# Kernel tuning notes

Hardware: AMD Instinct MI355X
Metric: run time of the kernel (lower is better)

Reference implementation:

```python
import jax, jax.numpy as jnp
import numpy as np

BN_EPS = 1e-3  # Keras BatchNormalization default epsilon


def _conv_block(x, k):
    """Per-task conv (stride 2, pad 1) -> ReLU -> BatchNorm (center/scale=False, training).

    x: [B, E, H, W, Cin]  (B tasks, E examples per task)
    k: [B, kh, kw, Cin, Cout]  per-task kernel
    """
    def conv_one(xe, kt):  # xe: [E,H,W,Cin], kt: [kh,kw,Cin,Cout]
        return jax.lax.conv_general_dilated(
            xe, kt, window_strides=(2, 2), padding=[(1, 1), (1, 1)],
            dimension_numbers=('NHWC', 'HWIO', 'NHWC'))
    y = jax.nn.relu(jax.vmap(conv_one)(x, k))  # [B,E,H',W',Cout]
    # BatchNorm in training mode: moments over all axes except channels
    m = jnp.mean(y, axis=(0, 1, 2, 3))
    v = jnp.var(y, axis=(0, 1, 2, 3))
    return (y - m) * jax.lax.rsqrt(v + BN_EPS)


def setup_inputs() -> dict:
    key = jax.random.key(0)
    ks = jax.random.split(key, 6)
    B, E, H, C, O = 64, 64, 28, 64, 20
    return {
        'x': jax.random.normal(ks[0], (B, E, H, H, 1), dtype=jnp.float32),
        'k1': jax.random.normal(ks[1], (B, 3, 3, 1, C), dtype=jnp.float32) * 0.1,
        'k2': jax.random.normal(ks[2], (B, 3, 3, C, C), dtype=jnp.float32) * 0.05,
        'k3': jax.random.normal(ks[3], (B, 3, 3, C, C), dtype=jnp.float32) * 0.05,
        'k4': jax.random.normal(ks[4], (B, 3, 3, C, C), dtype=jnp.float32) * 0.05,
        'w_ro': jax.random.normal(ks[5], (B, C, O), dtype=jnp.float32) * 0.1,
    }


def reference(x, k1, k2, k3, k4, w_ro):
    h = _conv_block(x, k1)   # [B,E,14,14,C]
    h = _conv_block(h, k2)   # [B,E,7,7,C]
    h = _conv_block(h, k3)   # [B,E,4,4,C]
    h = _conv_block(h, k4)   # [B,E,2,2,C]
    # MaxPooling2D with pool size == full spatial extent -> global spatial max
    feat = jnp.max(h, axis=(2, 3))  # [B,E,C]
    # per-task readout matmul: [B,E,H] x [B,H,O] -> [B,E,O]
    return jnp.einsum('beh,bho->beo', feat, w_ro)
```

## Files before the change

kernel.cpp:

```cpp
#include <hip/hip_runtime.h>

#define BN_EPS 1e-3f

typedef __attribute__((ext_vector_type(8))) short bf16x8;
typedef __attribute__((ext_vector_type(16))) float floatx16;
typedef unsigned short u16;

__device__ __forceinline__ u16 f2bf(float f) {
  unsigned u = __float_as_uint(f);
  u += 0x7fffu + ((u >> 16) & 1u);
  return (u16)(u >> 16);
}
__device__ __forceinline__ float bf2f(u16 h) {
  return __uint_as_float(((unsigned)h) << 16);
}

static constexpr int NSHARD = 64;

__global__ __launch_bounds__(256) void conv1_kernel(
    const float* __restrict__ x, const float* __restrict__ k1,
    u16* __restrict__ y1, float* __restrict__ statsSh)
{
  __shared__ float xp[900];
  __shared__ float w1[576];
  __shared__ float red[256];

  const int be = blockIdx.x, b = be >> 6, tid = threadIdx.x;

  for (int i = tid; i < 900; i += 256) xp[i] = 0.f;
  for (int i = tid; i < 576; i += 256) w1[i] = k1[(size_t)b * 576 + i];
  __syncthreads();
  for (int i = tid; i < 784; i += 256) {
    const int r = i / 28, cc = i - 28 * r;
    xp[(r + 1) * 30 + (cc + 1)] = x[(size_t)be * 784 + i];
  }
  __syncthreads();

  const int c = tid & 63;
  float wr[9];
#pragma unroll
  for (int t = 0; t < 9; ++t) wr[t] = w1[t * 64 + c];

  float sum = 0.f, ss = 0.f;
  for (int pix = tid >> 6; pix < 196; pix += 4) {
    const int oy = pix / 14, ox = pix - 14 * oy;
    const float* xb = &xp[(2 * oy) * 30 + 2 * ox];
    float acc = 0.f;
#pragma unroll
    for (int ky = 0; ky < 3; ++ky)
#pragma unroll
      for (int kx = 0; kx < 3; ++kx)
        acc = fmaf(xb[ky * 30 + kx], wr[ky * 3 + kx], acc);
    const float v = fmaxf(acc, 0.f);
    y1[((size_t)be * 196 + pix) * 64 + c] = f2bf(v);
    sum += v;
    ss = fmaf(v, v, ss);
  }

  red[tid] = sum;
  __syncthreads();
  if (tid < 64)
    atomicAdd(&statsSh[(blockIdx.x & (NSHARD - 1)) * 128 + tid],
              red[tid] + red[tid + 64] + red[tid + 128] + red[tid + 192]);
  __syncthreads();
  red[tid] = ss;
  __syncthreads();
  if (tid < 64)
    atomicAdd(&statsSh[(blockIdx.x & (NSHARD - 1)) * 128 + 64 + tid],
              red[tid] + red[tid + 64] + red[tid + 128] + red[tid + 192]);
}

__global__ __launch_bounds__(256) void fold_kernel(
    const float* __restrict__ W, const float* __restrict__ statsSh, float invN,
    u16* __restrict__ Wf, float* __restrict__ biasCls)
{
  __shared__ float T[64 * 68];
  __shared__ float P[256];
  __shared__ float s1[64], t1[64];
  __shared__ float tbS[64];

  const int b = blockIdx.x / 3, sg = blockIdx.x % 3;
  const int tid = threadIdx.x;

  {
    const int g = tid >> 7, cidx = tid & 127;
    float acc = 0.f;
    for (int k = 0; k < NSHARD / 2; ++k)
      acc += statsSh[(g * (NSHARD / 2) + k) * 128 + cidx];
    P[tid] = acc;
  }
  __syncthreads();
  if (tid < 64) {
    const float m = (P[tid] + P[tid + 128]) * invN;
    const float var = fmaf(-m, m, (P[64 + tid] + P[192 + tid]) * invN);
    const float s = rsqrtf(var + BN_EPS);
    s1[tid] = s;
    t1[tid] = -m * s;
  }
  __syncthreads();

  const int cin = tid >> 2, q0 = (tid & 3) * 16;
  const int cout = tid >> 2, ci0 = (tid & 3) * 16;
  for (int s = sg * 3; s < sg * 3 + 3; ++s) {
    if (tid < 64) tbS[tid] = 0.f;
    const float* ss = W + ((size_t)b * 9 + s) * 4096;
#pragma unroll
    for (int q = 0; q < 16; q += 4) {
      const float4 v = *(const float4*)(ss + cin * 64 + q0 + q);
      T[(q0 + q + 0) * 68 + cin] = v.x;
      T[(q0 + q + 1) * 68 + cin] = v.y;
      T[(q0 + q + 2) * 68 + cin] = v.z;
      T[(q0 + q + 3) * 68 + cin] = v.w;
    }
    __syncthreads();
    alignas(16) u16 tmp[16];
    float tb = 0.f;
#pragma unroll
    for (int j = 0; j < 16; ++j) {
      const float wv = T[cout * 68 + ci0 + j];
      tmp[j] = f2bf(wv * s1[ci0 + j]);
      tb = fmaf(t1[ci0 + j], wv, tb);
    }
    u16* dst = Wf + ((size_t)b * 9 + s) * 4096 + cout * 64 + ci0;
    *(uint4*)dst       = *(uint4*)&tmp[0];
    *(uint4*)(dst + 8) = *(uint4*)&tmp[8];
    atomicAdd(&tbS[cout], tb);
    __syncthreads();
    if (tid < 64) {
      const int ky = s / 3, kx = s % 3;
      const float tv = tbS[tid];
#pragma unroll
      for (int cls = 0; cls < 9; ++cls) {
        const int ry = cls / 3, rx = cls % 3;
        const bool valid = !((ry == 1 && ky == 0) || (ry == 2 && ky == 2) ||
                             (rx == 1 && kx == 0) || (rx == 2 && kx == 2));
        if (valid) atomicAdd(&biasCls[(size_t)b * 576 + cls * 64 + tid], tv);
      }
    }
    __syncthreads();
  }
}

template <int Hin, int Hout, int G>
__global__ __launch_bounds__(256) void conv_gemm_kernel(
    const u16* __restrict__ yin, const u16* __restrict__ Wf,
    const float* __restrict__ biasCls, u16* __restrict__ yout,
    float* __restrict__ statsSh)
{
  constexpr int PPI  = Hout * Hout;
  constexpr int ROWS = G * PPI;
  constexpr int BPT  = 64 / G;
  constexpr int LDA  = 68;

  __shared__ __align__(16) u16 AS[128 * LDA];
  __shared__ __align__(16) u16 BtS[64 * LDA];
  __shared__ float biasS[576];
  __shared__ float redsum[64], redss[64];

  const int b = blockIdx.x / BPT;
  const int e0 = (blockIdx.x % BPT) * G;
  const int tid = threadIdx.x, lane = tid & 63, wave = tid >> 6;

  for (int i = tid; i < 576; i += 256) biasS[i] = biasCls[(size_t)b * 576 + i];
  if (tid < 64) { redsum[tid] = 0.f; redss[tid] = 0.f; }

  const int arow = tid >> 1, ci0 = (tid & 1) * 32;
  const bool rowOk = arow < ROWS;
  const int g = rowOk ? arow / PPI : 0;
  const int pp = rowOk ? arow % PPI : 0;
  const int oy = pp / Hout, ox = pp % Hout;
  const size_t inBase = ((size_t)(b * 64 + e0 + g)) * (Hin * Hin) * 64;

  const int bco = tid >> 2, bci = (tid & 3) * 16;
  const u16* wbase = Wf + (size_t)b * 9 * 4096 + bco * 64 + bci;

  uint4 pa0, pa1, pa2, pa3, pb0, pb1;
  auto loadSlice = [&](int s) {
    const int ky = s / 3, kx = s % 3;
    const int iy = 2 * oy - 1 + ky, ix = 2 * ox - 1 + kx;
    if (rowOk && (unsigned)iy < (unsigned)Hin && (unsigned)ix < (unsigned)Hin) {
      const u16* src = yin + inBase + (size_t)(iy * Hin + ix) * 64 + ci0;
      pa0 = *(const uint4*)(src);
      pa1 = *(const uint4*)(src + 8);
      pa2 = *(const uint4*)(src + 16);
      pa3 = *(const uint4*)(src + 24);
    } else {
      pa0 = pa1 = pa2 = pa3 = uint4{0, 0, 0, 0};
    }
    const u16* wsl = wbase + s * 4096;
    pb0 = *(const uint4*)wsl;
    pb1 = *(const uint4*)(wsl + 8);
  };

  const int m0 = wave * 32;
  const int l31 = lane & 31;
  const int kq = (lane >> 5) * 8;

  floatx16 acc0, acc1;
#pragma unroll
  for (int r = 0; r < 16; ++r) { acc0[r] = 0.f; acc1[r] = 0.f; }

  loadSlice(0);
#pragma unroll
  for (int s = 0; s < 9; ++s) {
    *(uint4*)&AS[arow * LDA + ci0]      = pa0;
    *(uint4*)&AS[arow * LDA + ci0 + 8]  = pa1;
    *(uint4*)&AS[arow * LDA + ci0 + 16] = pa2;
    *(uint4*)&AS[arow * LDA + ci0 + 24] = pa3;
    *(uint4*)&BtS[bco * LDA + bci]     = pb0;
    *(uint4*)&BtS[bco * LDA + bci + 8] = pb1;
    __syncthreads();
    if (s < 8) loadSlice(s + 1);
#pragma unroll
    for (int kk = 0; kk < 4; ++kk) {
      const int ko = kk * 16 + kq;
      bf16x8 a  = *(const bf16x8*)&AS[(m0 + l31) * LDA + ko];
      bf16x8 b0 = *(const bf16x8*)&BtS[l31 * LDA + ko];
      bf16x8 b1 = *(const bf16x8*)&BtS[(32 + l31) * LDA + ko];
      acc0 = __builtin_amdgcn_mfma_f32_32x32x16_bf16(a, b0, acc0, 0, 0, 0);
      acc1 = __builtin_amdgcn_mfma_f32_32x32x16_bf16(a, b1, acc1, 0, 0, 0);
    }
    __syncthreads();
  }

  float ls0 = 0.f, lss0 = 0.f, ls1 = 0.f, lss1 = 0.f;
  const int col0 = l31, col1 = 32 + l31;
  const int rb = m0 + 4 * (lane >> 5);
#pragma unroll
  for (int r = 0; r < 16; ++r) {
    const int rw = rb + (r & 3) + 8 * (r >> 2);
    if (rw < ROWS) {
      const int re = rw / PPI, pr = rw % PPI;
      const int ooy = pr / Hout, oox = pr % Hout;
      const int ry = (ooy == 0) ? 1 : ((2 * ooy + 1 >= Hin) ? 2 : 0);
      const int rx = (oox == 0) ? 1 : ((2 * oox + 1 >= Hin) ? 2 : 0);
      const int cls = ry * 3 + rx;
      const size_t ob = ((size_t)(b * 64 + e0 + re) * PPI + pr) * 64;
      const float v0 = fmaxf(acc0[r] + biasS[cls * 64 + col0], 0.f);
      const float v1 = fmaxf(acc1[r] + biasS[cls * 64 + col1], 0.f);
      yout[ob + col0] = f2bf(v0);
      yout[ob + col1] = f2bf(v1);
      ls0 += v0; lss0 = fmaf(v0, v0, lss0);
      ls1 += v1; lss1 = fmaf(v1, v1, lss1);
    }
  }
  atomicAdd(&redsum[col0], ls0);
  atomicAdd(&redss[col0], lss0);
  atomicAdd(&redsum[col1], ls1);
  atomicAdd(&redss[col1], lss1);
  __syncthreads();
  if (tid < 64) {
    const int sh = blockIdx.x & (NSHARD - 1);
    atomicAdd(&statsSh[sh * 128 + tid], redsum[tid]);
    atomicAdd(&statsSh[sh * 128 + 64 + tid], redss[tid]);
  }
}

__global__ __launch_bounds__(256) void readout_kernel(
    const u16* __restrict__ y4, const float* __restrict__ w_ro,
    const float* __restrict__ statsSh, float invN, float* __restrict__ outp)
{
  __shared__ float wl[64 * 20];
  __shared__ float feat[64 * 64];
  __shared__ float P[256];
  __shared__ float sArr[64], tArr[64];

  const int b = blockIdx.x, tid = threadIdx.x;

  {
    const int g = tid >> 7, cidx = tid & 127;
    float acc = 0.f;
    for (int k = 0; k < NSHARD / 2; ++k)
      acc += statsSh[(g * (NSHARD / 2) + k) * 128 + cidx];
    P[tid] = acc;
  }
  for (int i = tid; i < 1280; i += 256) wl[i] = w_ro[(size_t)b * 1280 + i];
  __syncthreads();
  if (tid < 64) {
    const float m = (P[tid] + P[tid + 128]) * invN;
    const float var = fmaf(-m, m, (P[64 + tid] + P[192 + tid]) * invN);
    const float s = rsqrtf(var + BN_EPS);
    sArr[tid] = s;
    tArr[tid] = -m * s;
  }
  __syncthreads();

  {
    const int e = tid & 63;
    for (int c = tid >> 6; c < 64; c += 4) {
      const u16* p4 = y4 + ((size_t)(b * 64 + e) * 4) * 64 + c;
      const float v = fmaxf(fmaxf(bf2f(p4[0]), bf2f(p4[64])),
                            fmaxf(bf2f(p4[128]), bf2f(p4[192])));
      feat[c * 64 + e] = fmaf(v, sArr[c], tArr[c]);
    }
  }
  __syncthreads();

  const int e = tid >> 2, og = (tid & 3) * 5;
  float acc[5] = {0.f, 0.f, 0.f, 0.f, 0.f};
  for (int c = 0; c < 64; ++c) {
    const float f = feat[c * 64 + e];
#pragma unroll
    for (int j = 0; j < 5; ++j) acc[j] = fmaf(f, wl[c * 20 + og + j], acc[j]);
  }
#pragma unroll
  for (int j = 0; j < 5; ++j)
    outp[((size_t)b * 64 + e) * 20 + og + j] = acc[j];
}

extern "C" void kernel_launch(void* const* d_in, const int* in_sizes, int n_in,
                              void* d_out, int out_size, void* d_ws, size_t ws_size,
                              hipStream_t stream) {
  (void)in_sizes; (void)n_in; (void)out_size; (void)ws_size;
  const float* x   = (const float*)d_in[0];
  const float* k1  = (const float*)d_in[1];
  const float* k2  = (const float*)d_in[2];
  const float* k3  = (const float*)d_in[3];
  const float* k4  = (const float*)d_in[4];
  const float* wro = (const float*)d_in[5];
  float* out = (float*)d_out;
  char* ws = (char*)d_ws;

  float* stats = (float*)ws;
  float* bias2 = (float*)(ws + 131072);
  float* bias3 = bias2 + 36864;
  float* bias4 = bias3 + 36864;
  u16* k2f = (u16*)(ws + 131072 + 442368);
  u16* k3f = k2f + (size_t)2359296;
  u16* k4f = k3f + (size_t)2359296;
  u16* y2 = k4f + (size_t)2359296;
  u16* y1 = y2 + (size_t)12845056;
  u16* y3 = y1;
  u16* y4 = y3 + (size_t)4194304;

  float* st1 = stats;
  float* st2 = stats + 8192;
  float* st3 = stats + 16384;
  float* st4 = stats + 24576;

  hipMemsetAsync(stats, 0, 131072 + 442368, stream);

  conv1_kernel<<<4096, 256, 0, stream>>>(x, k1, y1, st1);
  fold_kernel<<<192, 256, 0, stream>>>(k2, st1, 1.f / 802816.f, k2f, bias2);
  conv_gemm_kernel<14, 7, 2><<<2048, 256, 0, stream>>>(y1, k2f, bias2, y2, st2);
  fold_kernel<<<192, 256, 0, stream>>>(k3, st2, 1.f / 200704.f, k3f, bias3);
  conv_gemm_kernel<7, 4, 8><<<512, 256, 0, stream>>>(y2, k3f, bias3, y3, st3);
  fold_kernel<<<192, 256, 0, stream>>>(k4, st3, 1.f / 65536.f, k4f, bias4);
  conv_gemm_kernel<4, 2, 32><<<128, 256, 0, stream>>>(y3, k4f, bias4, y4, st4);
  readout_kernel<<<64, 256, 0, stream>>>(y4, wro, st4, 1.f / 16384.f, out);
}
```

Before: 309.9 us.

## Stage whole input images in LDS for conv GEMMs and register-tile conv1

```diff
diff --git a/kernel.cpp b/kernel.cpp
--- a/kernel.cpp
+++ b/kernel.cpp
@@ -17,60 +17,74 @@
 
 static constexpr int NSHARD = 64;
 
-__global__ __launch_bounds__(256) void conv1_kernel(
+__global__ __launch_bounds__(256) void conv1_k(
     const float* __restrict__ x, const float* __restrict__ k1,
     u16* __restrict__ y1, float* __restrict__ statsSh)
 {
-  __shared__ float xp[900];
-  __shared__ float w1[576];
-  __shared__ float red[256];
+  __shared__ float xp[30 * 32];
+  __shared__ float w1s[576];
+  __shared__ float redsum[64], redss[64];
 
   const int be = blockIdx.x, b = be >> 6, tid = threadIdx.x;
 
-  for (int i = tid; i < 900; i += 256) xp[i] = 0.f;
-  for (int i = tid; i < 576; i += 256) w1[i] = k1[(size_t)b * 576 + i];
+  for (int i = tid; i < 960; i += 256) xp[i] = 0.f;
+  for (int i = tid; i < 576; i += 256) w1s[i] = k1[(size_t)b * 576 + i];
+  if (tid < 64) { redsum[tid] = 0.f; redss[tid] = 0.f; }
   __syncthreads();
   for (int i = tid; i < 784; i += 256) {
-    const int r = i / 28, cc = i - 28 * r;
-    xp[(r + 1) * 30 + (cc + 1)] = x[(size_t)be * 784 + i];
-  }
-  __syncthreads();
-
-  const int c = tid & 63;
-  float wr[9];
-#pragma unroll
-  for (int t = 0; t < 9; ++t) wr[t] = w1[t * 64 + c];
-
-  float sum = 0.f, ss = 0.f;
-  for (int pix = tid >> 6; pix < 196; pix += 4) {
-    const int oy = pix / 14, ox = pix - 14 * oy;
-    const float* xb = &xp[(2 * oy) * 30 + 2 * ox];
-    float acc = 0.f;
+    const int r = i / 28, c = i - 28 * r;
+    xp[(r + 1) * 32 + (c + 1)] = x[(size_t)be * 784 + i];
+  }
+  __syncthreads();
+
+  if (tid < 224) {
+    const int oy = tid >> 4, cg = (tid & 15) * 4;
+    float w[4][9];
+#pragma unroll
+    for (int cc = 0; cc < 4; ++cc)
+#pragma unroll
+      for (int t = 0; t < 9; ++t) w[cc][t] = w1s[t * 64 + cg + cc];
+
+    float xr[3][29];
 #pragma unroll
     for (int ky = 0; ky < 3; ++ky)
 #pragma unroll
-      for (int kx = 0; kx < 3; ++kx)
-        acc = fmaf(xb[ky * 30 + kx], wr[ky * 3 + kx], acc);
-    const float v = fmaxf(acc, 0.f);
-    y1[((size_t)be * 196 + pix) * 64 + c] = f2bf(v);
-    sum += v;
-    ss = fmaf(v, v, ss);
-  }
-
-  red[tid] = sum;
-  __syncthreads();
-  if (tid < 64)
-    atomicAdd(&statsSh[(blockIdx.x & (NSHARD - 1)) * 128 + tid],
-              red[tid] + red[tid + 64] + red[tid + 128] + red[tid + 192]);
-  __syncthreads();
-  red[tid] = ss;
-  __syncthreads();
-  if (tid < 64)
-    atomicAdd(&statsSh[(blockIdx.x & (NSHARD - 1)) * 128 + 64 + tid],
-              red[tid] + red[tid + 64] + red[tid + 128] + red[tid + 192]);
-}
-
-__global__ __launch_bounds__(256) void fold_kernel(
+      for (int j = 0; j < 29; ++j) xr[ky][j] = xp[(2 * oy + ky) * 32 + j];
+
+    float sum[4] = {0.f, 0.f, 0.f, 0.f}, ss[4] = {0.f, 0.f, 0.f, 0.f};
+#pragma unroll
+    for (int ox = 0; ox < 14; ++ox) {
+      alignas(8) u16 o[4];
+#pragma unroll
+      for (int cc = 0; cc < 4; ++cc) {
+        float a = 0.f;
+#pragma unroll
+        for (int ky = 0; ky < 3; ++ky)
+#pragma unroll
+          for (int kx = 0; kx < 3; ++kx)
+            a = fmaf(xr[ky][2 * ox + kx], w[cc][ky * 3 + kx], a);
+        const float v = fmaxf(a, 0.f);
+        o[cc] = f2bf(v);
+        sum[cc] += v;
+        ss[cc] = fmaf(v, v, ss[cc]);
+      }
+      *(uint2*)&y1[((size_t)be * 196 + oy * 14 + ox) * 64 + cg] = *(uint2*)o;
+    }
+#pragma unroll
+    for (int cc = 0; cc < 4; ++cc) {
+      atomicAdd(&redsum[cg + cc], sum[cc]);
+      atomicAdd(&redss[cg + cc], ss[cc]);
+    }
+  }
+  __syncthreads();
+  if (tid < 64) {
+    const int sh = be & (NSHARD - 1);
+    atomicAdd(&statsSh[sh * 128 + tid], redsum[tid]);
+    atomicAdd(&statsSh[sh * 128 + 64 + tid], redss[tid]);
+  }
+}
+
+__global__ __launch_bounds__(256) void foldw_k(
     const float* __restrict__ W, const float* __restrict__ statsSh, float invN,
     u16* __restrict__ Wf, float* __restrict__ biasCls)
 {
@@ -142,90 +156,94 @@
 }
 
 template <int Hin, int Hout, int G>
-__global__ __launch_bounds__(256) void conv_gemm_kernel(
+__device__ __forceinline__ void conv_core(
     const u16* __restrict__ yin, const u16* __restrict__ Wf,
     const float* __restrict__ biasCls, u16* __restrict__ yout,
-    float* __restrict__ statsSh)
+    float* __restrict__ statsSh, int blk)
 {
   constexpr int PPI  = Hout * Hout;
   constexpr int ROWS = G * PPI;
   constexpr int BPT  = 64 / G;
-  constexpr int LDA  = 68;
-
-  __shared__ __align__(16) u16 AS[128 * LDA];
-  __shared__ __align__(16) u16 BtS[64 * LDA];
+  constexpr int MR   = G * Hin * Hin;
+  constexpr int ZR   = MR;
+
+  __shared__ __align__(16) u16 mapS[(MR + 1) * 72];
+  __shared__ __align__(16) u16 Bb[2][64 * 72];
   __shared__ float biasS[576];
   __shared__ float redsum[64], redss[64];
 
-  const int b = blockIdx.x / BPT;
-  const int e0 = (blockIdx.x % BPT) * G;
+  const int b = blk / BPT, e0 = (blk % BPT) * G;
   const int tid = threadIdx.x, lane = tid & 63, wave = tid >> 6;
 
   for (int i = tid; i < 576; i += 256) biasS[i] = biasCls[(size_t)b * 576 + i];
   if (tid < 64) { redsum[tid] = 0.f; redss[tid] = 0.f; }
-
-  const int arow = tid >> 1, ci0 = (tid & 1) * 32;
-  const bool rowOk = arow < ROWS;
-  const int g = rowOk ? arow / PPI : 0;
-  const int pp = rowOk ? arow % PPI : 0;
+  if (tid < 8) *(uint4*)&mapS[ZR * 72 + tid * 8] = uint4{0, 0, 0, 0};
+
+  {
+    const u16* src = yin + (size_t)(b * 64 + e0) * (Hin * Hin) * 64;
+    for (int ch = tid; ch < MR * 8; ch += 256) {
+      const int r = ch >> 3, c8 = ch & 7;
+      *(uint4*)&mapS[r * 72 + c8 * 8] = *(const uint4*)(src + ch * 8);
+    }
+  }
+
+  const int bco = tid >> 2, bci = (tid & 3) * 16;
+  const u16* wb = Wf + (size_t)b * 9 * 4096 + bco * 64 + bci;
+  {
+    uint4 b0 = *(const uint4*)wb;
+    uint4 b1 = *(const uint4*)(wb + 8);
+    *(uint4*)&Bb[0][bco * 72 + bci]     = b0;
+    *(uint4*)&Bb[0][bco * 72 + bci + 8] = b1;
+  }
+
+  const int m0 = (wave & 1) * 32, n0 = (wave >> 1) * 32;
+  const int l31 = lane & 31, kq = (lane >> 5) * 8;
+  const int lrow = m0 + l31;
+  const bool rv = lrow < ROWS;
+  const int img = rv ? lrow / PPI : 0;
+  const int pp  = rv ? lrow % PPI : 0;
   const int oy = pp / Hout, ox = pp % Hout;
-  const size_t inBase = ((size_t)(b * 64 + e0 + g)) * (Hin * Hin) * 64;
-
-  const int bco = tid >> 2, bci = (tid & 3) * 16;
-  const u16* wbase = Wf + (size_t)b * 9 * 4096 + bco * 64 + bci;
-
-  uint4 pa0, pa1, pa2, pa3, pb0, pb1;
-  auto loadSlice = [&](int s) {
+
+  floatx16 acc;
+#pragma unroll
+  for (int r = 0; r < 16; ++r) acc[r] = 0.f;
+
+  __syncthreads();
+
+#pragma unroll
+  for (int s = 0; s < 9; ++s) {
+    uint4 nb0, nb1;
+    if (s < 8) {
+      const u16* wsl = wb + (s + 1) * 4096;
+      nb0 = *(const uint4*)wsl;
+      nb1 = *(const uint4*)(wsl + 8);
+    }
     const int ky = s / 3, kx = s % 3;
-    const int iy = 2 * oy - 1 + ky, ix = 2 * ox - 1 + kx;
-    if (rowOk && (unsigned)iy < (unsigned)Hin && (unsigned)ix < (unsigned)Hin) {
-      const u16* src = yin + inBase + (size_t)(iy * Hin + ix) * 64 + ci0;
-      pa0 = *(const uint4*)(src);
-      pa1 = *(const uint4*)(src + 8);
-      pa2 = *(const uint4*)(src + 16);
-      pa3 = *(const uint4*)(src + 24);
-    } else {
-      pa0 = pa1 = pa2 = pa3 = uint4{0, 0, 0, 0};
-    }
-    const u16* wsl = wbase + s * 4096;
-    pb0 = *(const uint4*)wsl;
-    pb1 = *(const uint4*)(wsl + 8);
-  };
-
-  const int m0 = wave * 32;
-  const int l31 = lane & 31;
-  const int kq = (lane >> 5) * 8;
-
-  floatx16 acc0, acc1;
-#pragma unroll
-  for (int r = 0; r < 16; ++r) { acc0[r] = 0.f; acc1[r] = 0.f; }
-
-  loadSlice(0);
-#pragma unroll
-  for (int s = 0; s < 9; ++s) {
-    *(uint4*)&AS[arow * LDA + ci0]      = pa0;
-    *(uint4*)&AS[arow * LDA + ci0 + 8]  = pa1;
-    *(uint4*)&AS[arow * LDA + ci0 + 16] = pa2;
-    *(uint4*)&AS[arow * LDA + ci0 + 24] = pa3;
-    *(uint4*)&BtS[bco * LDA + bci]     = pb0;
-    *(uint4*)&BtS[bco * LDA + bci + 8] = pb1;
+    int pix = ZR;
+    if (rv) {
+      const int iy = 2 * oy - 1 + ky, ix = 2 * ox - 1 + kx;
+      if ((unsigned)iy < (unsigned)Hin && (unsigned)ix < (unsigned)Hin)
+        pix = img * (Hin * Hin) + iy * Hin + ix;
+    }
+    const u16* ap = &mapS[pix * 72 + kq];
+    const u16* bp = &Bb[s & 1][(n0 + l31) * 72 + kq];
+#pragma unroll
+    for (int kk = 0; kk < 4; ++kk) {
+      bf16x8 a  = *(const bf16x8*)(ap + kk * 16);
+      bf16x8 bv = *(const bf16x8*)(bp + kk * 16);
+      acc = __builtin_amdgcn_mfma_f32_32x32x16_bf16(a, bv, acc, 0, 0, 0);
+    }
+    if (s < 8) {
+      u16* d = &Bb[(s + 1) & 1][bco * 72 + bci];
+      *(uint4*)d       = nb0;
+      *(uint4*)(d + 8) = nb1;
+    }
     __syncthreads();
-    if (s < 8) loadSlice(s + 1);
-#pragma unroll
-    for (int kk = 0; kk < 4; ++kk) {
-      const int ko = kk * 16 + kq;
-      bf16x8 a  = *(const bf16x8*)&AS[(m0 + l31) * LDA + ko];
-      bf16x8 b0 = *(const bf16x8*)&BtS[l31 * LDA + ko];
-      bf16x8 b1 = *(const bf16x8*)&BtS[(32 + l31) * LDA + ko];
-      acc0 = __builtin_amdgcn_mfma_f32_32x32x16_bf16(a, b0, acc0, 0, 0, 0);
-      acc1 = __builtin_amdgcn_mfma_f32_32x32x16_bf16(a, b1, acc1, 0, 0, 0);
-    }
-    __syncthreads();
-  }
-
-  float ls0 = 0.f, lss0 = 0.f, ls1 = 0.f, lss1 = 0.f;
-  const int col0 = l31, col1 = 32 + l31;
+  }
+
+  const int col = n0 + l31;
   const int rb = m0 + 4 * (lane >> 5);
+  float ls = 0.f, lss = 0.f;
 #pragma unroll
   for (int r = 0; r < 16; ++r) {
     const int rw = rb + (r & 3) + 8 * (r >> 2);
@@ -234,29 +252,42 @@
       const int ooy = pr / Hout, oox = pr % Hout;
       const int ry = (ooy == 0) ? 1 : ((2 * ooy + 1 >= Hin) ? 2 : 0);
       const int rx = (oox == 0) ? 1 : ((2 * oox + 1 >= Hin) ? 2 : 0);
-      const int cls = ry * 3 + rx;
-      const size_t ob = ((size_t)(b * 64 + e0 + re) * PPI + pr) * 64;
-      const float v0 = fmaxf(acc0[r] + biasS[cls * 64 + col0], 0.f);
-      const float v1 = fmaxf(acc1[r] + biasS[cls * 64 + col1], 0.f);
-      yout[ob + col0] = f2bf(v0);
-      yout[ob + col1] = f2bf(v1);
-      ls0 += v0; lss0 = fmaf(v0, v0, lss0);
-      ls1 += v1; lss1 = fmaf(v1, v1, lss1);
-    }
-  }
-  atomicAdd(&redsum[col0], ls0);
-  atomicAdd(&redss[col0], lss0);
-  atomicAdd(&redsum[col1], ls1);
-  atomicAdd(&redss[col1], lss1);
+      const float v = fmaxf(acc[r] + biasS[(ry * 3 + rx) * 64 + col], 0.f);
+      yout[((size_t)(b * 64 + e0 + re) * PPI + pr) * 64 + col] = f2bf(v);
+      ls += v;
+      lss = fmaf(v, v, lss);
+    }
+  }
+  atomicAdd(&redsum[col], ls);
+  atomicAdd(&redss[col], lss);
   __syncthreads();
   if (tid < 64) {
-    const int sh = blockIdx.x & (NSHARD - 1);
+    const int sh = blk & (NSHARD - 1);
     atomicAdd(&statsSh[sh * 128 + tid], redsum[tid]);
     atomicAdd(&statsSh[sh * 128 + 64 + tid], redss[tid]);
   }
 }
 
-__global__ __launch_bounds__(256) void readout_kernel(
+__global__ __launch_bounds__(256) void cg2_k(
+    const u16* __restrict__ yin, const u16* __restrict__ Wf,
+    const float* __restrict__ biasCls, u16* __restrict__ yout,
+    float* __restrict__ statsSh) {
+  conv_core<14, 7, 1>(yin, Wf, biasCls, yout, statsSh, blockIdx.x);
+}
+__global__ __launch_bounds__(256) void cg3_k(
+    const u16* __restrict__ yin, const u16* __restrict__ Wf,
+    const float* __restrict__ biasCls, u16* __restrict__ yout,
+    float* __restrict__ statsSh) {
+  conv_core<7, 4, 4>(yin, Wf, biasCls, yout, statsSh, blockIdx.x);
+}
+__global__ __launch_bounds__(256) void cg4_k(
+    const u16* __restrict__ yin, const u16* __restrict__ Wf,
+    const float* __restrict__ biasCls, u16* __restrict__ yout,
+    float* __restrict__ statsSh) {
+  conv_core<4, 2, 16>(yin, Wf, biasCls, yout, statsSh, blockIdx.x);
+}
+
+__global__ __launch_bounds__(256) void readout_k(
     const u16* __restrict__ y4, const float* __restrict__ w_ro,
     const float* __restrict__ statsSh, float invN, float* __restrict__ outp)
 {
@@ -340,12 +371,12 @@
 
   hipMemsetAsync(stats, 0, 131072 + 442368, stream);
 
-  conv1_kernel<<<4096, 256, 0, stream>>>(x, k1, y1, st1);
-  fold_kernel<<<192, 256, 0, stream>>>(k2, st1, 1.f / 802816.f, k2f, bias2);
-  conv_gemm_kernel<14, 7, 2><<<2048, 256, 0, stream>>>(y1, k2f, bias2, y2, st2);
-  fold_kernel<<<192, 256, 0, stream>>>(k3, st2, 1.f / 200704.f, k3f, bias3);
-  conv_gemm_kernel<7, 4, 8><<<512, 256, 0, stream>>>(y2, k3f, bias3, y3, st3);
-  fold_kernel<<<192, 256, 0, stream>>>(k4, st3, 1.f / 65536.f, k4f, bias4);
-  conv_gemm_kernel<4, 2, 32><<<128, 256, 0, stream>>>(y3, k4f, bias4, y4, st4);
-  readout_kernel<<<64, 256, 0, stream>>>(y4, wro, st4, 1.f / 16384.f, out);
-}
+  conv1_k<<<4096, 256, 0, stream>>>(x, k1, y1, st1);
+  foldw_k<<<192, 256, 0, stream>>>(k2, st1, 1.f / 802816.f, k2f, bias2);
+  cg2_k<<<4096, 256, 0, stream>>>(y1, k2f, bias2, y2, st2);
+  foldw_k<<<192, 256, 0, stream>>>(k3, st2, 1.f / 200704.f, k3f, bias3);
+  cg3_k<<<1024, 256, 0, stream>>>(y2, k3f, bias3, y3, st3);
+  foldw_k<<<192, 256, 0, stream>>>(k4, st3, 1.f / 65536.f, k4f, bias4);
+  cg4_k<<<256, 256, 0, stream>>>(y3, k4f, bias4, y4, st4);
+  readout_k<<<64, 256, 0, stream>>>(y4, wro, st4, 1.f / 16384.f, out);
+}
```

Measured after the change: 265.3 us. -14.4%, faster.
